# Performance work log

Hardware: AMD Instinct MI355X
Metric: run time of the kernel (lower is better)

Reference implementation:

```python
import jax, jax.numpy as jnp
import numpy as np

GAMMA = 0.99  # init kwarg


def _discounted_returns(ep_rs):
    # reversed running_add = running_add*gamma + r, emitted per step
    def step(carry, r):
        carry = carry * GAMMA + r
        return carry, carry
    _, out = jax.lax.scan(step, jnp.float32(0.0), ep_rs, reverse=True)
    return out  # [T]


def setup_inputs() -> dict:
    key = jax.random.key(0)
    k1, k2, k3 = jax.random.split(key, 3)
    T, A = 2097152, 18
    weight = jax.random.normal(k1, (T, A), dtype=jnp.float32)
    ep_rs = jax.random.normal(k2, (T,), dtype=jnp.float32)
    ep_as = jax.random.randint(k3, (T,), 0, A, dtype=jnp.int64)
    return {"weight": weight, "ep_rs": ep_rs, "ep_as": ep_as}


def reference(weight, ep_rs, ep_as):
    d = _discounted_returns(ep_rs)
    d = d - jnp.mean(d)
    # cross_entropy with reduction='none': -log_softmax(weight)[t, ep_as[t]]
    logp = jax.nn.log_softmax(weight, axis=-1)  # [T, A]
    neg_log_prob = -jnp.take_along_axis(logp, ep_as[:, None], axis=-1)[:, 0]  # [T]
    return jnp.mean(neg_log_prob * d)
```

## Files before the change

kernel.cpp:

```cpp
#include <hip/hip_runtime.h>
#include <math.h>

#define T_TOTAL 2097152
#define A_DIM   18
#define GAMMA_D 0.99

#define CHUNK 256
#define NC    (T_TOTAL / CHUNK)
#define KTR   14
#define CPB   4
#define NB    (NC / CPB)

__global__ __launch_bounds__(256, 4)
void k_mega(const float* __restrict__ wgt, const int* __restrict__ act,
            const float* __restrict__ r, double* __restrict__ partials) {
    __shared__ double ldsL[17];
    __shared__ double ldsD[CPB * CHUNK];
    __shared__ double red[12];
    const int tid  = threadIdx.x;
    const int lane = tid & 63, wv = tid >> 6;
    const int c0   = blockIdx.x * CPB;
    const double g  = GAMMA_D;
    const double G_ = pow(g, 256.0);
    const double w4 = pow(g, (double)(4 * lane));

    const size_t rowBase = (size_t)c0 * CHUNK;
    const float4* wp0 = (const float4*)(wgt + (rowBase + 2 * (size_t)tid) * A_DIM);
    float4 a0[9];
    #pragma unroll
    for (int q = 0; q < 9; ++q) a0[q] = wp0[q];
    const int2 aa0 = *(const int2*)(act + rowBase + 2 * tid);

    #pragma unroll
    for (int i = 0; i < 5; ++i) {
        const int k  = wv + 4 * i;
        const int cc = c0 + 1 + k;
        if (k < 17) {
            double val = 0.0;
            if (cc < NC) {
                const float4 v = ((const float4*)r)[(size_t)cc * 64 + lane];
                val = w4 * ((double)v.x + g * ((double)v.y + g * ((double)v.z + g * (double)v.w)));
                #pragma unroll
                for (int off = 32; off > 0; off >>= 1) val += __shfl_down(val, off, 64);
            }
            if (lane == 0) ldsL[k] = val;
        }
    }
    __syncthreads();

    {
        double acc = 0.0, wG = 1.0;
        #pragma unroll
        for (int m = 0; m < KTR; ++m) { acc += wG * ldsL[wv + m]; wG *= G_; }
        const int c = c0 + wv;
        const float4 v = ((const float4*)r)[(size_t)c * 64 + lane];
        const double u3 = (double)v.w;
        const double u2 = (double)v.z + g * u3;
        const double u1 = (double)v.y + g * u2;
        const double u0 = (double)v.x + g * u1;
        double S = w4 * u0;
        #pragma unroll
        for (int off = 1; off < 64; off <<= 1) {
            const double t = __shfl_down(S, off, 64);
            S += (lane + off < 64) ? t : 0.0;
        }
        double Snext = __shfl_down(S, 1, 64);
        if (lane == 63) Snext = 0.0;
        const double A  = (1.0 / w4) * (Snext + G_ * acc);
        const double ig = 1.0 / g;
        double* dp = ldsD + wv * CHUNK + 4 * lane;
        dp[0] = u0 + A;
        dp[1] = u1 + ig * A;
        dp[2] = u2 + (ig * ig) * A;
        dp[3] = u3 + (ig * ig * ig) * A;
    }
    __syncthreads();

    const float4* wp1 = (const float4*)(wgt + (rowBase + 512 + 2 * (size_t)tid) * A_DIM);
    float4 a1[9];
    #pragma unroll
    for (int q = 0; q < 9; ++q) a1[q] = wp1[q];
    const int2    aa1 = *(const int2*)(act + rowBase + 512 + 2 * tid);
    const double2 dd0 = *(const double2*)(ldsD + 2 * tid);
    const double2 dd1 = *(const double2*)(ldsD + 512 + 2 * tid);

    double s_n = 0.0, s_nd = 0.0;
    double s_d = dd0.x + dd0.y + dd1.x + dd1.y;
    float w[36];
    #pragma unroll
    for (int q = 0; q < 9; ++q) {
        w[4*q+0] = a0[q].x; w[4*q+1] = a0[q].y; w[4*q+2] = a0[q].z; w[4*q+3] = a0[q].w;
    }
    {
        float mx = w[0];
        #pragma unroll
        for (int j = 1; j < A_DIM; ++j) mx = fmaxf(mx, w[j]);
        float s = 0.0f, wsel = 0.0f;
        #pragma unroll
        for (int j = 0; j < A_DIM; ++j) { s += expf(w[j] - mx); wsel = (j == aa0.x) ? w[j] : wsel; }
        const float nlp = mx + logf(s) - wsel;
        s_n += (double)nlp;  s_nd += (double)nlp * dd0.x;
    }
    {
        float mx = w[18];
        #pragma unroll
        for (int j = 1; j < A_DIM; ++j) mx = fmaxf(mx, w[18 + j]);
        float s = 0.0f, wsel = 0.0f;
        #pragma unroll
        for (int j = 0; j < A_DIM; ++j) { s += expf(w[18 + j] - mx); wsel = (j == aa0.y) ? w[18 + j] : wsel; }
        const float nlp = mx + logf(s) - wsel;
        s_n += (double)nlp;  s_nd += (double)nlp * dd0.y;
    }
    #pragma unroll
    for (int q = 0; q < 9; ++q) {
        w[4*q+0] = a1[q].x; w[4*q+1] = a1[q].y; w[4*q+2] = a1[q].z; w[4*q+3] = a1[q].w;
    }
    {
        float mx = w[0];
        #pragma unroll
        for (int j = 1; j < A_DIM; ++j) mx = fmaxf(mx, w[j]);
        float s = 0.0f, wsel = 0.0f;
        #pragma unroll
        for (int j = 0; j < A_DIM; ++j) { s += expf(w[j] - mx); wsel = (j == aa1.x) ? w[j] : wsel; }
        const float nlp = mx + logf(s) - wsel;
        s_n += (double)nlp;  s_nd += (double)nlp * dd1.x;
    }
    {
        float mx = w[18];
        #pragma unroll
        for (int j = 1; j < A_DIM; ++j) mx = fmaxf(mx, w[18 + j]);
        float s = 0.0f, wsel = 0.0f;
        #pragma unroll
        for (int j = 0; j < A_DIM; ++j) { s += expf(w[18 + j] - mx); wsel = (j == aa1.y) ? w[18 + j] : wsel; }
        const float nlp = mx + logf(s) - wsel;
        s_n += (double)nlp;  s_nd += (double)nlp * dd1.y;
    }

    #pragma unroll
    for (int off = 32; off > 0; off >>= 1) {
        s_d  += __shfl_down(s_d,  off, 64);
        s_n  += __shfl_down(s_n,  off, 64);
        s_nd += __shfl_down(s_nd, off, 64);
    }
    if (lane == 0) { red[wv*3+0] = s_d; red[wv*3+1] = s_n; red[wv*3+2] = s_nd; }
    __syncthreads();
    if (tid == 0) {
        double a = 0.0, b = 0.0, cc = 0.0;
        #pragma unroll
        for (int q = 0; q < 4; ++q) { a += red[q*3]; b += red[q*3+1]; cc += red[q*3+2]; }
        partials[blockIdx.x*3+0] = a;
        partials[blockIdx.x*3+1] = b;
        partials[blockIdx.x*3+2] = cc;
    }
}

__global__ void k_final(const double* __restrict__ partials, float* __restrict__ out) {
    __shared__ double red[12];
    const int tid = threadIdx.x;
    double a = 0.0, b = 0.0, c = 0.0;
    for (int i = tid; i < NB; i += 256) {
        a += partials[i*3+0];
        b += partials[i*3+1];
        c += partials[i*3+2];
    }
    #pragma unroll
    for (int off = 32; off > 0; off >>= 1) {
        a += __shfl_down(a, off, 64);
        b += __shfl_down(b, off, 64);
        c += __shfl_down(c, off, 64);
    }
    const int lane = tid & 63, wv = tid >> 6;
    if (lane == 0) { red[wv*3+0] = a; red[wv*3+1] = b; red[wv*3+2] = c; }
    __syncthreads();
    if (tid == 0) {
        double A_ = 0.0, B_ = 0.0, C_ = 0.0;
        #pragma unroll
        for (int i = 0; i < 4; ++i) { A_ += red[i*3]; B_ += red[i*3+1]; C_ += red[i*3+2]; }
        const double invT = 1.0 / (double)T_TOTAL;
        out[0] = (float)((C_ - (A_ * invT) * B_) * invT);
    }
}

extern "C" void kernel_launch(void* const* d_in, const int* in_sizes, int n_in,
                              void* d_out, int out_size, void* d_ws, size_t ws_size,
                              hipStream_t stream) {
    const float* weight = (const float*)d_in[0];
    const float* ep_rs  = (const float*)d_in[1];
    const int*   ep_as  = (const int*)  d_in[2];
    float* out = (float*)d_out;

    double* partials = (double*)d_ws;

    k_mega  <<<NB, 256, 0, stream>>>(weight, ep_as, ep_rs, partials);
    k_final <<<1,  256, 0, stream>>>(partials, out);
}
```

Measured before the change: 232.6 us.

## Fuse final reduction via atomics and last-block flag; prefetch reward windows early

```diff
diff --git a/kernel.cpp b/kernel.cpp
--- a/kernel.cpp
+++ b/kernel.cpp
@@ -10,10 +10,12 @@
 #define KTR   14
 #define CPB   4
 #define NB    (NC / CPB)
+#define BLK   256
 
-__global__ __launch_bounds__(256, 4)
+__global__ __launch_bounds__(BLK, 4)
 void k_mega(const float* __restrict__ wgt, const int* __restrict__ act,
-            const float* __restrict__ r, double* __restrict__ partials) {
+            const float* __restrict__ r, double* __restrict__ acc,
+            unsigned int* __restrict__ flag, float* __restrict__ out) {
     __shared__ double ldsL[17];
     __shared__ double ldsD[CPB * CHUNK];
     __shared__ double red[12];
@@ -24,6 +26,17 @@
     const double G_ = pow(g, 256.0);
     const double w4 = pow(g, (double)(4 * lane));
 
+    float4 rwin[5];
+    #pragma unroll
+    for (int i = 0; i < 5; ++i) {
+        const int k  = wv + 4 * i;
+        const int cc = c0 + 1 + k;
+        rwin[i] = (k < 17 && cc < NC)
+                  ? ((const float4*)r)[(size_t)cc * 64 + lane]
+                  : make_float4(0, 0, 0, 0);
+    }
+    const float4 rown = ((const float4*)r)[(size_t)(c0 + wv) * 64 + lane];
+
     const size_t rowBase = (size_t)c0 * CHUNK;
     const float4* wp0 = (const float4*)(wgt + (rowBase + 2 * (size_t)tid) * A_DIM);
     float4 a0[9];
@@ -33,31 +46,25 @@
 
     #pragma unroll
     for (int i = 0; i < 5; ++i) {
-        const int k  = wv + 4 * i;
-        const int cc = c0 + 1 + k;
+        const int k = wv + 4 * i;
         if (k < 17) {
-            double val = 0.0;
-            if (cc < NC) {
-                const float4 v = ((const float4*)r)[(size_t)cc * 64 + lane];
-                val = w4 * ((double)v.x + g * ((double)v.y + g * ((double)v.z + g * (double)v.w)));
-                #pragma unroll
-                for (int off = 32; off > 0; off >>= 1) val += __shfl_down(val, off, 64);
-            }
+            double val = w4 * ((double)rwin[i].x + g * ((double)rwin[i].y +
+                         g * ((double)rwin[i].z + g * (double)rwin[i].w)));
+            #pragma unroll
+            for (int off = 32; off > 0; off >>= 1) val += __shfl_down(val, off, 64);
             if (lane == 0) ldsL[k] = val;
         }
     }
     __syncthreads();
 
     {
-        double acc = 0.0, wG = 1.0;
+        double acc_c = 0.0, wG = 1.0;
         #pragma unroll
-        for (int m = 0; m < KTR; ++m) { acc += wG * ldsL[wv + m]; wG *= G_; }
-        const int c = c0 + wv;
-        const float4 v = ((const float4*)r)[(size_t)c * 64 + lane];
-        const double u3 = (double)v.w;
-        const double u2 = (double)v.z + g * u3;
-        const double u1 = (double)v.y + g * u2;
-        const double u0 = (double)v.x + g * u1;
+        for (int m = 0; m < KTR; ++m) { acc_c += wG * ldsL[wv + m]; wG *= G_; }
+        const double u3 = (double)rown.w;
+        const double u2 = (double)rown.z + g * u3;
+        const double u1 = (double)rown.y + g * u2;
+        const double u0 = (double)rown.x + g * u1;
         double S = w4 * u0;
         #pragma unroll
         for (int off = 1; off < 64; off <<= 1) {
@@ -66,7 +73,7 @@
         }
         double Snext = __shfl_down(S, 1, 64);
         if (lane == 63) Snext = 0.0;
-        const double A  = (1.0 / w4) * (Snext + G_ * acc);
+        const double A  = (1.0 / w4) * (Snext + G_ * acc_c);
         const double ig = 1.0 / g;
         double* dp = ldsD + wv * CHUNK + 4 * lane;
         dp[0] = u0 + A;
@@ -145,39 +152,22 @@
     if (lane == 0) { red[wv*3+0] = s_d; red[wv*3+1] = s_n; red[wv*3+2] = s_nd; }
     __syncthreads();
     if (tid == 0) {
-        double a = 0.0, b = 0.0, cc = 0.0;
+        double pa = 0.0, pb = 0.0, pc = 0.0;
         #pragma unroll
-        for (int q = 0; q < 4; ++q) { a += red[q*3]; b += red[q*3+1]; cc += red[q*3+2]; }
-        partials[blockIdx.x*3+0] = a;
-        partials[blockIdx.x*3+1] = b;
-        partials[blockIdx.x*3+2] = cc;
-    }
-}
-
-__global__ void k_final(const double* __restrict__ partials, float* __restrict__ out) {
-    __shared__ double red[12];
-    const int tid = threadIdx.x;
-    double a = 0.0, b = 0.0, c = 0.0;
-    for (int i = tid; i < NB; i += 256) {
-        a += partials[i*3+0];
-        b += partials[i*3+1];
-        c += partials[i*3+2];
-    }
-    #pragma unroll
-    for (int off = 32; off > 0; off >>= 1) {
-        a += __shfl_down(a, off, 64);
-        b += __shfl_down(b, off, 64);
-        c += __shfl_down(c, off, 64);
-    }
-    const int lane = tid & 63, wv = tid >> 6;
-    if (lane == 0) { red[wv*3+0] = a; red[wv*3+1] = b; red[wv*3+2] = c; }
-    __syncthreads();
-    if (tid == 0) {
-        double A_ = 0.0, B_ = 0.0, C_ = 0.0;
-        #pragma unroll
-        for (int i = 0; i < 4; ++i) { A_ += red[i*3]; B_ += red[i*3+1]; C_ += red[i*3+2]; }
-        const double invT = 1.0 / (double)T_TOTAL;
-        out[0] = (float)((C_ - (A_ * invT) * B_) * invT);
+        for (int q = 0; q < 4; ++q) { pa += red[q*3]; pb += red[q*3+1]; pc += red[q*3+2]; }
+        atomicAdd(&acc[0], pa);
+        atomicAdd(&acc[1], pb);
+        atomicAdd(&acc[2], pc);
+        __threadfence();
+        const unsigned int old = atomicAdd(flag, 1u);
+        if (old == NB - 1) {
+            __threadfence();
+            const double sd  = atomicAdd(&acc[0], 0.0);
+            const double sn  = atomicAdd(&acc[1], 0.0);
+            const double snd = atomicAdd(&acc[2], 0.0);
+            const double invT = 1.0 / (double)T_TOTAL;
+            out[0] = (float)((snd - (sd * invT) * sn) * invT);
+        }
     }
 }
 
@@ -189,8 +179,9 @@
     const int*   ep_as  = (const int*)  d_in[2];
     float* out = (float*)d_out;
 
-    double* partials = (double*)d_ws;
+    double*       acc  = (double*)d_ws;
+    unsigned int* flag = (unsigned int*)((char*)d_ws + 24);
 
-    k_mega  <<<NB, 256, 0, stream>>>(weight, ep_as, ep_rs, partials);
-    k_final <<<1,  256, 0, stream>>>(partials, out);
+    hipMemsetAsync(d_ws, 0, 64, stream);
+    k_mega<<<NB, BLK, 0, stream>>>(weight, ep_as, ep_rs, acc, flag, out);
 }
```

Result: slower. 322.6 us (+38.7%).
